# Kernel tuning notes

Measured on AMD Instinct MI355X. Metric: run time of the kernel, lower is better.

The kernel has to match this reference:

```python
import jax, jax.numpy as jnp
import numpy as np

B, T, H, CD, NC, S, D = 128, 256, 512, 128, 2048, 256, 9
EPS = 1e-5

def _lin(x, w, b):
    return x @ w.T + b

def _gru_cell(x, h, wih, whh, bih, bhh):
    gi = x @ wih.T + bih
    gh = h @ whh.T + bhh
    ir, iz, inn = jnp.split(gi, 3, axis=-1)
    hr, hz, hn = jnp.split(gh, 3, axis=-1)
    r = jax.nn.sigmoid(ir + hr)
    z = jax.nn.sigmoid(iz + hz)
    n = jnp.tanh(inn + r * hn)
    return (1.0 - z) * n + z * h

def _bn(x, g, b, m, v):
    # eval-mode BatchNorm1d over channel dim of [B,C,W]
    return (x - m[:, None]) * (g * jax.lax.rsqrt(v + EPS))[:, None] + b[:, None]

def _conv(x, w, b, stride, pad):
    y = jax.lax.conv_general_dilated(x, w, (stride,), [(pad, pad)], dimension_numbers=('NCW', 'OIW', 'NCW'))
    return y + b[:, None]

def _convT(x, w, b, stride, pad, out_pad):
    # torch ConvTranspose1d with weight [I,O,k] == dilated conv with flipped, transposed kernel
    k = w.shape[-1]
    w2 = jnp.flip(w, -1).transpose(1, 0, 2)  # [O,I,k]
    y = jax.lax.conv_general_dilated(x, w2, (1,), [(k - 1 - pad, k - 1 - pad + out_pad)], lhs_dilation=(stride,), dimension_numbers=('NCW', 'OIW', 'NCW'))
    return y + b[:, None]

def _gru_seq(x, h0, wih, whh, bih, bhh, reverse=False):
    def step(h, xt):
        hn = _gru_cell(xt, h, wih, whh, bih, bhh)
        return hn, hn
    _, ys = jax.lax.scan(step, h0, jnp.swapaxes(x, 0, 1), reverse=reverse)
    return jnp.swapaxes(ys, 0, 1)

def _forward(note, skel, skel_encoded, ehw, ehb, ifw, ifb, gfwih, gfwhh, gfbih, gfbhh, gbwih, gbwhh, gbbih, gbbhh, bn0g, bn0b, bn0m, bn0v, c1w, c1b, bn1g, bn1b, bn1m, bn1v, c2w, c2b, bn2g, bn2b, bn2m, bn2v, c3w, c3b, embed, ct1w, ct1b, dbn1g, dbn1b, dbn1m, dbn1v, ct2w, ct2b, dbn2g, dbn2b, dbn2m, dbn2v, dhw, dhb, g1wih, g1whh, g1bih, g1bhh, g2wih, g2whh, g2bih, g2bhh, nfw, nfb, samp_rand):
    sg = jax.lax.stop_gradient
    # ---- encoder ----
    hid = _lin(skel_encoded, ehw, ehb)                         # [B,H] shared init for both GRU dirs
    x = _lin(note, ifw, ifb)                                   # [B,T,H]
    fwd = _gru_seq(x, hid, gfwih, gfwhh, gfbih, gfbhh)
    bwd = _gru_seq(x, hid, gbwih, gbwhh, gbbih, gbbhh, reverse=True)
    out = jnp.concatenate([fwd, bwd], axis=-1).transpose(0, 2, 1)  # [B,2H,T]
    out = _bn(out, bn0g, bn0b, bn0m, bn0v)
    out = jax.nn.leaky_relu(_bn(_conv(out, c1w, c1b, 2, 1), bn1g, bn1b, bn1m, bn1v), 0.2)
    out = jax.nn.leaky_relu(_bn(_conv(out, c2w, c2b, 2, 1), bn2g, bn2b, bn2m, bn2v), 0.2)
    z = _conv(out, c3w, c3b, 1, 0)                             # [B,CD,T//4]
    # ---- vector quantizer (eval: no EMA update) ----
    zt = z.transpose(0, 2, 1)                                  # [B,T//4,CD]
    flat = zt.reshape(-1, CD)
    dist = (flat * flat).sum(1, keepdims=True) - 2.0 * flat @ embed.T + (embed * embed).sum(1)
    idx = jnp.argmin(dist, axis=1)                             # [B*T//4]
    quant = embed[idx].reshape(zt.shape)
    codebook_loss = jnp.mean((sg(quant) - zt) ** 2)
    cmt_loss = jnp.mean((quant - sg(zt)) ** 2)
    loss = codebook_loss + 0.2 * cmt_loss
    quant_st = zt + sg(quant - zt)                             # straight-through
    qz = quant_st.transpose(0, 2, 1)                           # [B,CD,T//4]
    avg_probs = jnp.zeros((NC,), zt.dtype).at[idx].add(1.0) / idx.shape[0]
    perplexity = jnp.exp(-jnp.sum(avg_probs * jnp.log(avg_probs + 1e-10)))
    enc_idx = idx.reshape(B, -1, 1)
    # ---- decoder ----
    d = jax.nn.leaky_relu(_bn(_convT(qz, ct1w, ct1b, 2, 0, 1), dbn1g, dbn1b, dbn1m, dbn1v), 0.2)
    d = jax.nn.leaky_relu(_bn(_convT(d, ct2w, ct2b, 2, 0, 0), dbn2g, dbn2b, dbn2m, dbn2v), 0.2)
    dec_in = d.transpose(0, 2, 1)                              # [B,T+8,H//2]
    h1 = _lin(skel_encoded, dhw, dhb)
    out0 = jnp.zeros((B, D), zt.dtype)
    cat0 = jnp.concatenate([out0, dec_in[:, 0], skel[:, 0]], axis=-1)
    h1 = _gru_cell(cat0, h1, g1wih, g1whh, g1bih, g1bhh)
    h2 = _gru_cell(h1, h1, g2wih, g2whh, g2bih, g2bhh)         # hx[1] init = hx[0] at i==0
    logit0 = _lin(h2, nfw, nfb)
    fb0 = (jax.nn.sigmoid(logit0) - samp_rand[0] > 0).astype(zt.dtype)  # eval-mode bernoulli sample
    def step(carry, xs):
        fb, h1, h2 = carry
        inp_i, skel_i, rand_i = xs
        h1 = _gru_cell(jnp.concatenate([fb, inp_i, skel_i], axis=-1), h1, g1wih, g1whh, g1bih, g1bhh)
        h2 = _gru_cell(h1, h2, g2wih, g2whh, g2bih, g2bhh)
        logits = _lin(h2, nfw, nfb)
        fb = (jax.nn.sigmoid(logits) - rand_i > 0).astype(logits.dtype)
        return (fb, h1, h2), logits
    xs = (jnp.swapaxes(dec_in[:, 1:T], 0, 1), jnp.swapaxes(skel[:, 1:T], 0, 1), samp_rand[1:T])
    _, logits_rest = jax.lax.scan(step, (fb0, h1, h2), xs)
    note_recon = jnp.swapaxes(jnp.concatenate([logit0[None], logits_rest], axis=0), 0, 1)  # [B,T,D]
    return note_recon, qz, loss, cmt_loss, enc_idx, perplexity

def setup_inputs():
    key = jax.random.key(0)
    ks = iter(jax.random.split(key, 96))
    nrm = lambda *s: jax.random.normal(next(ks), s, jnp.float32) * 0.05
    uni = lambda *s: jax.random.uniform(next(ks), s, jnp.float32)
    def bnp(c):
        g = 1.0 + 0.1 * jax.random.normal(next(ks), (c,), jnp.float32)
        b = nrm(c)
        m = nrm(c) * 2.0
        v = jax.random.uniform(next(ks), (c,), jnp.float32, 0.5, 1.5)
        return g, b, m, v
    inp = {}
    inp['note'] = uni(B, T, D)
    inp['skel'] = uni(B, T, D)
    inp['skel_encoded'] = jax.random.normal(next(ks), (B, S), jnp.float32)
    inp['ehw'] = nrm(H, S); inp['ehb'] = nrm(H)
    inp['ifw'] = nrm(H, D); inp['ifb'] = nrm(H)
    inp['gfwih'] = nrm(3 * H, H); inp['gfwhh'] = nrm(3 * H, H); inp['gfbih'] = nrm(3 * H); inp['gfbhh'] = nrm(3 * H)
    inp['gbwih'] = nrm(3 * H, H); inp['gbwhh'] = nrm(3 * H, H); inp['gbbih'] = nrm(3 * H); inp['gbbhh'] = nrm(3 * H)
    inp['bn0g'], inp['bn0b'], inp['bn0m'], inp['bn0v'] = bnp(2 * H)
    inp['c1w'] = nrm(H, 2 * H, 4); inp['c1b'] = nrm(H)
    inp['bn1g'], inp['bn1b'], inp['bn1m'], inp['bn1v'] = bnp(H)
    inp['c2w'] = nrm(H, H, 4); inp['c2b'] = nrm(H)
    inp['bn2g'], inp['bn2b'], inp['bn2m'], inp['bn2v'] = bnp(H)
    inp['c3w'] = nrm(CD, H, 1); inp['c3b'] = nrm(CD)
    inp['embed'] = jax.random.normal(next(ks), (NC, CD), jnp.float32)  # torch normal_() init, std 1
    inp['ct1w'] = nrm(CD, H, 4); inp['ct1b'] = nrm(H)
    inp['dbn1g'], inp['dbn1b'], inp['dbn1m'], inp['dbn1v'] = bnp(H)
    inp['ct2w'] = nrm(H, H // 2, 4); inp['ct2b'] = nrm(H // 2)
    inp['dbn2g'], inp['dbn2b'], inp['dbn2m'], inp['dbn2v'] = bnp(H // 2)
    inp['dhw'] = nrm(H, S); inp['dhb'] = nrm(H)
    inp['g1wih'] = nrm(3 * H, H // 2 + 2 * D); inp['g1whh'] = nrm(3 * H, H); inp['g1bih'] = nrm(3 * H); inp['g1bhh'] = nrm(3 * H)
    inp['g2wih'] = nrm(3 * H, H); inp['g2whh'] = nrm(3 * H, H); inp['g2bih'] = nrm(3 * H); inp['g2bhh'] = nrm(3 * H)
    inp['nfw'] = nrm(D, H); inp['nfb'] = nrm(D)
    inp['samp_rand'] = uni(T, B, D)  # pre-drawn noise for eval-mode bernoulli sampling
    inp['training'] = 0
    inp['teacher_forcing_ratio'] = 0
    return inp

def reference(note, skel, skel_encoded, ehw, ehb, ifw, ifb, gfwih, gfwhh, gfbih, gfbhh, gbwih, gbwhh, gbbih, gbbhh, bn0g, bn0b, bn0m, bn0v, c1w, c1b, bn1g, bn1b, bn1m, bn1v, c2w, c2b, bn2g, bn2b, bn2m, bn2v, c3w, c3b, embed, ct1w, ct1b, dbn1g, dbn1b, dbn1m, dbn1v, ct2w, ct2b, dbn2g, dbn2b, dbn2m, dbn2v, dhw, dhb, g1wih, g1whh, g1bih, g1bhh, g2wih, g2whh, g2bih, g2bhh, nfw, nfb, samp_rand, training, teacher_forcing_ratio):
    # eval path: training flag unused (dropout off, BN running stats, no EMA, always sample)
    return _forward(note, skel, skel_encoded, ehw, ehb, ifw, ifb, gfwih, gfwhh, gfbih, gfbhh, gbwih, gbwhh, gbbih, gbbhh, bn0g, bn0b, bn0m, bn0v, c1w, c1b, bn1g, bn1b, bn1m, bn1v, c2w, c2b, bn2g, bn2b, bn2m, bn2v, c3w, c3b, embed, ct1w, ct1b, dbn1g, dbn1b, dbn1m, dbn1v, ct2w, ct2b, dbn2g, dbn2b, dbn2m, dbn2v, dhw, dhb, g1wih, g1whh, g1bih, g1bhh, g2wih, g2whh, g2bih, g2bhh, nfw, nfb, samp_rand)
```

## Files before the change

kernel.cpp:

```cpp
#include <hip/hip_runtime.h>
#include <math.h>


#define DI __device__ __forceinline__

#define O_HF   ((size_t)0)
#define O_HB   ((size_t)131072)
#define O_H1   ((size_t)262144)
#define O_H2   ((size_t)393216)
#define O_WEFF ((size_t)524288)
#define O_BEFF ((size_t)551936)
#define O_BNS  ((size_t)555008)
#define O_ESQ  ((size_t)560640)
#define O_HIST ((size_t)562688)
#define O_RED  ((size_t)564736)
#define O_LOG  ((size_t)564752)
#define O_IDX  ((size_t)567056)
#define O_ZT   ((size_t)575248)
#define O_QT   ((size_t)1623824)
#define O_C2   ((size_t)2672400)
#define O_C1   ((size_t)6866704)
#define O_WT1  ((size_t)15255312)
#define O_WT2  ((size_t)17352464)
#define O_WT3  ((size_t)18401040)
// ... 51 lines not shown
  C0 = MF(A1,Q1,C0); C1 = MF(A1,Q0,C1); \
  C0 = MF(A0,Q2,C0); C1 = MF(A2,Q0,C1); \
  C0 = MF(A2,Q1,C0); C1 = MF(A1,Q2,C1);

#define FMA44 \
  acc[0][0] += a4.x*b4.x; acc[0][1] += a4.x*b4.y; acc[0][2] += a4.x*b4.z; acc[0][3] += a4.x*b4.w; \
  acc[1][0] += a4.y*b4.x; acc[1][1] += a4.y*b4.y; acc[1][2] += a4.y*b4.z; acc[1][3] += a4.y*b4.w; \
  acc[2][0] += a4.z*b4.x; acc[2][1] += a4.z*b4.y; acc[2][2] += a4.z*b4.z; acc[2][3] += a4.z*b4.w; \
  acc[3][0] += a4.w*b4.x; acc[3][1] += a4.w*b4.y; acc[3][2] += a4.w*b4.z; acc[3][3] += a4.w*b4.w;

__global__ void trans_kern(const float* __restrict__ c1w, const float* __restrict__ c2w,
                           const float* __restrict__ c3w, const float* __restrict__ ct1w,
                           const float* __restrict__ ct2w, float* __restrict__ ws){
  const int A1 = 2097152, A2 = 3145728, A3 = 3211264, A4 = 3473408, A5 = 3997696;
  for (int i = blockIdx.x*256 + threadIdx.x; i < A5; i += gridDim.x*256){
    if (i < A1){
      int j = i; int oc = j & 511; int t = j >> 9; int ic = t & 1023; int k = t >> 10;
      ws[O_WT1 + j] = c1w[((size_t)oc*1024 + ic)*4 + k];
    } else if (i < A2){
      int j = i - A1; int oc = j & 511; int t = j >> 9; int ic = t & 511; int k = t >> 9;
      ws[O_WT2 + j] = c2w[((size_t)oc*512 + ic)*4 + k];
    } else if (i < A3){
      int j = i - A2; int oc = j & 127; int ic = j >> 7;
      ws[O_WT3 + j] = c3w[(size_t)oc*512 + ic];
    } else if (i < A4){
      int j = i - A3; int oc = j & 511; int t = j >> 9; int ic = t & 127; int k = t >> 7;
      ws[O_WTD1 + j] = ct1w[((size_t)ic*512 + oc)*4 + k];
    } else {
      int j = i - A4; int oc = j & 255; int t = j >> 8; int ic = t & 511; int k = t >> 9;
      ws[O_WTD2 + j] = ct2w[((size_t)ic*256 + oc)*4 + k];
    }
  }
}

__global__ void bn_kern(const float* g0,const float* b0,const float* m0,const float* v0,
                        const float* g1,const float* b1,const float* m1,const float* v1,
                        const float* g2,const float* b2,const float* m2,const float* v2,
                        const float* gd1,const float* bd1,const float* md1,const float* vd1,
                        const float* gd2,const float* bd2,const float* md2,const float* vd2,
                        float* __restrict__ bns){
  int i = blockIdx.x*256 + threadIdx.x;
  if (i >= 2816) return;
  const float *g,*b,*m,*v; int c, so, to;
  if (i < 1024){ g=g0;b=b0;m=m0;v=v0;c=i;so=BN0S;to=BN0T; }
  else if (i < 1536){ g=g1;b=b1;m=m1;v=v1;c=i-1024;so=BN1S;to=BN1T; }
  else if (i < 2048){ g=g2;b=b2;m=m2;v=v2;c=i-1536;so=BN2S;to=BN2T; }
  else if (i < 2560){ g=gd1;b=bd1;m=md1;v=vd1;c=i-2048;so=DB1S;to=DB1T; }
  else              { g=gd2;b=bd2;m=md2;v=vd2;c=i-2560;so=DB2S;to=DB2T; }
  float s = g[c]*rsqrtf(v[c] + 1e-5f);
  bns[so + c] = s;
  bns[to + c] = b[c] - m[c]*s;
}

__global__ __launch_bounds__(256) void init_kern(const float* __restrict__ se,
    const float* __restrict__ ehw, const float* __restrict__ ehb,
    const float* __restrict__ dhw, const float* __restrict__ dhb, float* __restrict__ ws){
  int idx = blockIdx.x*256 + threadIdx.x;
  int n = idx & 1023, b = idx >> 10;
  const float* w; float bias;
  if (n < 512){ w = ehw + (size_t)n*256; bias = ehb[n]; }
  else        { w = dhw + (size_t)(n-512)*256; bias = dhb[n-512]; }
  const float* sp = se + (size_t)b*256;
  float acc = bias;
  for (int k = 0; k < 256; ++k) acc += sp[k]*w[k];
  if (n < 512){
    ws[O_HF + 65536 + b*512 + n] = acc;
    ws[O_HB + 65536 + b*512 + n] = acc;
    unsigned short s0,s1,s2; split3(acc, s0,s1,s2);
    unsigned short* esh = (unsigned short*)(ws + ESOFF) + 4718592;
    int off = 196608 + b*512 + n;
    esh[off] = s0; esh[off+65536] = s1; esh[off+131072] = s2;
    esh[393216+off] = s0; esh[393216+off+65536] = s1; esh[393216+off+131072] = s2;
  } else {
    ws[O_H1 + 65536 + b*512 + (n-512)] = acc;
  }
}

__global__ __launch_bounds__(256) void weff_kern(const float* __restrict__ gfwih,
    const float* __restrict__ gfbih, const float* __restrict__ gbwih, const float* __restrict__ gbbih,
    const float* __restrict__ ifw, const float* __restrict__ ifb, float* __restrict__ ws){
  int idx = blockIdx.x*256 + threadIdx.x;
  if (idx >= 30720) return;
  int dir = idx / 15360; int r = idx - dir*15360;
  int j3 = r / 10; int d = r - j3*10;
  const float* wih = dir ? gbwih : gfwih;
  float acc = 0.f;
  if (d < 9){
    for (int k = 0; k < 512; ++k) acc += wih[(size_t)j3*512 + k]*ifw[k*9 + d];
    ws[O_WEFF + dir*13824 + j3*9 + d] = acc;
  } else {
    for (int k = 0; k < 512; ++k) acc += wih[(size_t)j3*512 + k]*ifb[k];
    acc += (dir ? gbbih : gfbih)[j3];
    ws[O_BEFF + dir*1536 + j3] = acc;
  }
}

__global__ __launch_bounds__(256) void esq_kern(const float* __restrict__ embed, float* __restrict__ ws){
  int e = blockIdx.x*256 + threadIdx.x;
  float acc = 0.f;
  for (int c = 0; c < 128; ++c){ float t = embed[(size_t)e*128 + c]; acc += t*t; }
  ws[O_ESQ + e] = acc;
  if (blockIdx.x == 0){
    for (int i = threadIdx.x; i < 2048; i += 256) ws[O_HIST + i] = 0.f;
    if (threadIdx.x < 16) ws[O_RED + threadIdx.x] = 0.f;
  }
}

__global__ void split_w_kern(const float* __restrict__ gfwhh,
    const float* __restrict__ gbwhh, float* __restrict__ ws){
  unsigned short* es = (unsigned short*)(ws + ESOFF);
  for (int i = blockIdx.x*256 + threadIdx.x; i < 1572864; i += gridDim.x*256){
    int half = i >= 786432;
    int idx = i - (half ? 786432 : 0);
    float x = half ? gbwhh[idx] : gfwhh[idx];
    unsigned short s0,s1,s2; split3(x,s0,s1,s2);
    unsigned short* d = es + (half ? 2359296 : 0);
    d[idx] = s0; d[idx+786432] = s1; d[idx+1572864] = s2;
  }
}

__global__ void split_w2_kern(const float* __restrict__ g1wih, const float* __restrict__ g1whh,
    const float* __restrict__ g2wih, const float* __restrict__ g2whh, float* __restrict__ ws){
  unsigned short* dsb = (unsigned short*)(ws + DSOFF);
  const int total = 393216 + 3*786432 + 65536;
  for (int i = blockIdx.x*256 + threadIdx.x; i < total; i += gridDim.x*256){
    float x; unsigned short* d; int off, stride;
    if (i < 393216){
      int row = i>>8, k = i&255;
      x = g1wih[(size_t)row*274 + 9 + k]; d = dsb; off = i; stride = 393216;
    } else if (i < 1179648){
      int idx = i-393216; x = g1whh[idx]; d = dsb + 1179648; off = idx; stride = 786432;
    } else if (i < 1966080){
      int idx = i-1179648; x = g2wih[idx]; d = dsb + 3538944; off = idx; stride = 786432;
    } else if (i < 2752512){
      int idx = i-1966080; x = g2whh[idx]; d = dsb + 5898240; off = idx; stride = 786432;
    } else {
      int idx = i-2752512; x = ws[O_H1 + 65536 + idx];
      d = dsb + 8257536 + 196608; off = idx; stride = 65536;
    }
    unsigned short s0,s1,s2; split3(x,s0,s1,s2);
    d[off] = s0; d[off+stride] = s1; d[off+2*stride] = s2;
  }
}

__global__ void split_dec_kern(float* __restrict__ ws){
  unsigned short* decs = (unsigned short*)(ws + ESOFF);
  const float* dec = ws + O_DEC;
  for (int i = blockIdx.x*256 + threadIdx.x; i < 8388608; i += gridDim.x*256){
    unsigned short s0,s1,s2; split3(dec[i],s0,s1,s2);
    decs[i] = s0; decs[i+8388608] = s1; decs[i+16777216] = s2;
  }
}

__global__ __launch_bounds__(256) void enc_step_mfma(
    float* __restrict__ ws, const float* __restrict__ note,
    const float* __restrict__ gfbhh, const float* __restrict__ gbbhh, int step){
  int bi = blockIdx.x;
  int dir = bi>>7, bt = (bi>>5)&3, jt = bi&31;
  int b0 = bt*32, j0 = jt*16;
  int tid = threadIdx.x, w = tid>>6, l = tid&63;
  int m = w&1, kh = w>>1;
  int pb = (step+1)&1, cb = step&1;
  float* hprev = ws + (dir? O_HB : O_HF) + (size_t)pb*65536;
  float* hnext = ws + (dir? O_HB : O_HF) + (size_t)cb*65536;
  unsigned short* esh = (unsigned short*)(ws + ESOFF) + 4718592 + dir*393216;
  const unsigned short* hsp = esh + pb*196608;
  unsigned short* hsn = esh + cb*196608;
  const unsigned short* wsp = (const unsigned short*)(ws + ESOFF) + dir*2359296;
  const float* weff = ws + O_WEFF + dir*13824;
  const float* beff = ws + O_BEFF + dir*1536;
  const float* bhh = dir? gbbhh : gfbhh;
  const float* bns = ws + O_BNS;
  float* ys = ws + O_YS;

  const unsigned short* ab = hsp + (b0 + m*16 + (l&15))*512 + kh*256 + ((l>>4)<<3);
  const unsigned short* bb = wsp + (j0 + (l&15))*512 + kh*256 + ((l>>4)<<3);
  f32x4 z4 = {0.f,0.f,0.f,0.f};
  f32x4 acc[3][2] = {{z4,z4},{z4,z4},{z4,z4}};
  #pragma unroll
  for (int kt = 0; kt < 8; ++kt){
    s8v a0 = LD8(ab + kt*32);
    s8v a1 = LD8(ab + 65536 + kt*32);
    s8v a2 = LD8(ab + 131072 + kt*32);
    #pragma unroll
    for (int g = 0; g < 3; ++g){
      const unsigned short* bp = bb + g*262144 + kt*32;
      s8v q0 = LD8(bp);
      s8v q1 = LD8(bp + 786432);
      s8v q2 = LD8(bp + 1572864);
      MF8(a0,a1,a2, q0,q1,q2, acc[g][0], acc[g][1])
    }
  }
  __shared__ float red[3072];
  #pragma unroll
  for (int g = 0; g < 3; ++g){
    f32x4 s = acc[g][0] + acc[g][1];
    #pragma unroll
    for (int i = 0; i < 4; ++i) red[((w*3+g)<<8) + (i<<6) + l] = s[i];
  }
  __syncthreads();
  int t = dir ? 255-step : step;
  #pragma unroll
  for (int ii = 0; ii < 2; ++ii){
    int i = kh*2 + ii;
    int b = b0 + m*16 + ((l>>4)<<2) + i;
    int j = j0 + (l&15);
    float Y[3];
    #pragma unroll
    for (int g = 0; g < 3; ++g)
      Y[g] = red[((m*3+g)<<8)+(i<<6)+l] + red[((m*3+g+6)<<8)+(i<<6)+l];
    const float* nt = note + ((size_t)b*256 + t)*9;
    float gi[3];
    #pragma unroll
    for (int g = 0; g < 3; ++g){
      const float* wr = weff + (size_t)(g*512+j)*9;
      float a = beff[g*512+j];
      #pragma unroll
      for (int d = 0; d < 9; ++d) a += nt[d]*wr[d];
      gi[g] = a;
    }
    float hpv = hprev[(size_t)b*512 + j];
    float r = sigm(gi[0] + Y[0] + bhh[j]);
    float zz = sigm(gi[1] + Y[1] + bhh[512+j]);
    float nn = tanhf(gi[2] + r*(Y[2] + bhh[1024+j]));
    float h = (1.f - zz)*nn + zz*hpv;
    hnext[(size_t)b*512 + j] = h;
    unsigned short s0,s1,s2; split3(h, s0,s1,s2);
    int off = b*512 + j;
    hsn[off] = s0; hsn[off+65536] = s1; hsn[off+131072] = s2;
    int c = dir*512 + j;
    ys[((size_t)b*256 + t)*1024 + c] = h*bns[BN0S + c] + bns[BN0T + c];
  }
}

__global__ __launch_bounds__(256) void dec_k1_mfma(
    float* __restrict__ ws, const float* __restrict__ skel, const float* __restrict__ sr,
    const float* __restrict__ w1ih, const float* __restrict__ b1ih,
    const float* __restrict__ b1hh, const float* __restrict__ nfb,
    float* __restrict__ dout, int step){
  int bi = blockIdx.x;
  int bt = bi>>5, jt = bi&31;
  int b0 = bt*16, j0 = jt*16;
  int tid = threadIdx.x, w = tid>>6, l = tid&63;
  int kh = w;
  int pb = (step+1)&1, cb = step&1;
  const float* h1p = ws + O_H1 + (size_t)pb*65536;
  float* h1n = ws + O_H1 + (size_t)cb*65536;
  const float* logp = ws + O_LOG + (size_t)pb*1152;
  float* logc = ws + O_LOG + (size_t)cb*1152;
  unsigned short* dsb = (unsigned short*)(ws + DSOFF);
  const unsigned short* h1sp = dsb + 8257536 + pb*196608;
  unsigned short* h1sn = dsb + 8257536 + cb*196608;
  const unsigned short* decs = (const unsigned short*)(ws + ESOFF);
  const unsigned short* w1d = dsb;
  const unsigned short* w1h = dsb + 1179648;

  __shared__ float fbs[144], ssh[144];
  __shared__ float red[6144];
  if (tid < 144){
    int bb = tid/9, d = tid - bb*9; int b = b0 + bb;
    float fv = 0.f;
    if (step > 0){
      float lg = logp[b*9 + d];
      fv = (1.f/(1.f + expf(-lg)) - sr[(size_t)(step-1)*1152 + b*9 + d]) > 0.f ? 1.f : 0.f;
    }
    fbs[tid] = fv;
    ssh[tid] = skel[((size_t)b*256 + step)*9 + d];
  }
  if (bi == 0){
    for (int idx = tid; idx < 1152; idx += 256){
      logc[idx] = nfb[idx % 9];
      if (step > 0) dout[OUT_NR + (size_t)(idx/9)*2304 + (step-1)*9 + (idx%9)] = logp[idx];
    }
  }
  f32x4 z4 = {0.f,0.f,0.f,0.f};
  f32x4 gia[3][2] = {{z4,z4},{z4,z4},{z4,z4}};
  f32x4 gha[3][2] = {{z4,z4},{z4,z4},{z4,z4}};
  {
    const unsigned short* ab = decs + (b0 + (l&15))*65536 + step*256 + kh*64 + ((l>>4)<<3);
    const unsigned short* bb = w1d + (j0 + (l&15))*256 + kh*64 + ((l>>4)<<3);
    #pragma unroll
    for (int kt = 0; kt < 2; ++kt){
      s8v a0 = LD8(ab + kt*32);
      s8v a1 = LD8(ab + 8388608 + kt*32);
      s8v a2 = LD8(ab + 16777216 + kt*32);
      #pragma unroll
      for (int g = 0; g < 3; ++g){
        const unsigned short* bp = bb + g*131072 + kt*32;
        s8v q0 = LD8(bp);
        s8v q1 = LD8(bp + 393216);
        s8v q2 = LD8(bp + 786432);
        MF8(a0,a1,a2, q0,q1,q2, gia[g][0], gia[g][1])
      }
    }
  }
  {
    const unsigned short* ab = h1sp + (b0 + (l&15))*512 + kh*128 + ((l>>4)<<3);
    const unsigned short* bb = w1h + (j0 + (l&15))*512 + kh*128 + ((l>>4)<<3);
    #pragma unroll
    for (int kt = 0; kt < 4; ++kt){
      s8v a0 = LD8(ab + kt*32);
      s8v a1 = LD8(ab + 65536 + kt*32);
      s8v a2 = LD8(ab + 131072 + kt*32);
      #pragma unroll
      for (int g = 0; g < 3; ++g){
        const unsigned short* bp = bb + g*262144 + kt*32;
        s8v q0 = LD8(bp);
        s8v q1 = LD8(bp + 786432);
        s8v q2 = LD8(bp + 1572864);
        MF8(a0,a1,a2, q0,q1,q2, gha[g][0], gha[g][1])
      }
    }
  }
  #pragma unroll
  for (int g = 0; g < 3; ++g){
    f32x4 s = gia[g][0] + gia[g][1];
    f32x4 t = gha[g][0] + gha[g][1];
    #pragma unroll
    for (int i = 0; i < 4; ++i){
      red[((w*6+g)<<8) + (i<<6) + l] = s[i];
      red[((w*6+g+3)<<8) + (i<<6) + l] = t[i];
    }
  }
  __syncthreads();
  int i = w;
  int b = b0 + ((l>>4)<<2) + i;
  int j = j0 + (l&15);
  float GI[3], GH[3];
  #pragma unroll
  for (int pg = 0; pg < 3; ++pg){
    float a = 0.f, c = 0.f;
    #pragma unroll
    for (int ww = 0; ww < 4; ++ww){
      a += red[((ww*6+pg)<<8)+(i<<6)+l];
      c += red[((ww*6+pg+3)<<8)+(i<<6)+l];
    }
    GI[pg] = a; GH[pg] = c;
  }
  int bb = b - b0;
  #pragma unroll
  for (int g = 0; g < 3; ++g){
    const float* wr = w1ih + (size_t)(g*512+j)*274;
    float a = GI[g] + b1ih[g*512+j];
    #pragma unroll
    for (int d = 0; d < 9; ++d) a += fbs[bb*9+d]*wr[d] + ssh[bb*9+d]*wr[265+d];
    GI[g] = a;
  }
  float hpv = h1p[(size_t)b*512 + j];
  float r = sigm(GI[0] + GH[0] + b1hh[j]);
  float zz = sigm(GI[1] + GH[1] + b1hh[512+j]);
  float nn = tanhf(GI[2] + r*(GH[2] + b1hh[1024+j]));
  float h = (1.f-zz)*nn + zz*hpv;
  h1n[(size_t)b*512 + j] = h;
  unsigned short s0,s1,s2; split3(h,s0,s1,s2);
  int off = b*512 + j;
  h1sn[off] = s0; h1sn[off+65536] = s1; h1sn[off+131072] = s2;
}

__global__ __launch_bounds__(256) void dec_k2_mfma(
    float* __restrict__ ws, const float* __restrict__ b2ih, const float* __restrict__ b2hh,
    const float* __restrict__ nfw, int step){
  int bi = blockIdx.x;
  int bt = bi>>5, jt = bi&31;
  int b0 = bt*16, j0 = jt*16;
  int tid = threadIdx.x, w = tid>>6, l = tid&63;
  int kh = w;
  int pb = (step+1)&1, cb = step&1;
  const float* h1n = ws + O_H1 + (size_t)cb*65536;
  const float* h2p = (step==0) ? h1n : ws + O_H2 + (size_t)pb*65536;
  float* h2n = ws + O_H2 + (size_t)cb*65536;
  float* logc = ws + O_LOG + (size_t)cb*1152;
  unsigned short* dsb = (unsigned short*)(ws + DSOFF);
  const unsigned short* h1sn = dsb + 8257536 + cb*196608;
  const unsigned short* h2sp = (step==0) ? h1sn : dsb + 8650752 + pb*196608;
  unsigned short* h2sn = dsb + 8650752 + cb*196608;
  const unsigned short* w2i = dsb + 3538944;
  const unsigned short* w2h = dsb + 5898240;

  __shared__ float red[6144];
  __shared__ float hsm[256];
  f32x4 z4 = {0.f,0.f,0.f,0.f};
  f32x4 gia[3][2] = {{z4,z4},{z4,z4},{z4,z4}};
  f32x4 gha[3][2] = {{z4,z4},{z4,z4},{z4,z4}};
  {
    const unsigned short* ab = h1sn + (b0 + (l&15))*512 + kh*128 + ((l>>4)<<3);
    const unsigned short* bb = w2i + (j0 + (l&15))*512 + kh*128 + ((l>>4)<<3);
    #pragma unroll
    for (int kt = 0; kt < 4; ++kt){
      s8v a0 = LD8(ab + kt*32);
      s8v a1 = LD8(ab + 65536 + kt*32);
      s8v a2 = LD8(ab + 131072 + kt*32);
      #pragma unroll
      for (int g = 0; g < 3; ++g){
        const unsigned short* bp = bb + g*262144 + kt*32;
        s8v q0 = LD8(bp);
        s8v q1 = LD8(bp + 786432);
        s8v q2 = LD8(bp + 1572864);
        MF8(a0,a1,a2, q0,q1,q2, gia[g][0], gia[g][1])
      }
    }
  }
  {
    const unsigned short* ab = h2sp + (b0 + (l&15))*512 + kh*128 + ((l>>4)<<3);
    const unsigned short* bb = w2h + (j0 + (l&15))*512 + kh*128 + ((l>>4)<<3);
    #pragma unroll
    for (int kt = 0; kt < 4; ++kt){
      s8v a0 = LD8(ab + kt*32);
      s8v a1 = LD8(ab + 65536 + kt*32);
      s8v a2 = LD8(ab + 131072 + kt*32);
      #pragma unroll
      for (int g = 0; g < 3; ++g){
        const unsigned short* bp = bb + g*262144 + kt*32;
        s8v q0 = LD8(bp);
        s8v q1 = LD8(bp + 786432);
        s8v q2 = LD8(bp + 1572864);
        MF8(a0,a1,a2, q0,q1,q2, gha[g][0], gha[g][1])
      }
    }
  }
  #pragma unroll
  for (int g = 0; g < 3; ++g){
    f32x4 s = gia[g][0] + gia[g][1];
    f32x4 t = gha[g][0] + gha[g][1];
    #pragma unroll
    for (int i = 0; i < 4; ++i){
      red[((w*6+g)<<8) + (i<<6) + l] = s[i];
      red[((w*6+g+3)<<8) + (i<<6) + l] = t[i];
    }
  }
  __syncthreads();
  int i = w;
  int b = b0 + ((l>>4)<<2) + i;
  int j = j0 + (l&15);
  float GI[3], GH[3];
  #pragma unroll
  for (int pg = 0; pg < 3; ++pg){
    float a = 0.f, c = 0.f;
    #pragma unroll
    for (int ww = 0; ww < 4; ++ww){
      a += red[((ww*6+pg)<<8)+(i<<6)+l];
      c += red[((ww*6+pg+3)<<8)+(i<<6)+l];
    }
    GI[pg] = a; GH[pg] = c;
  }
  float hpv = h2p[(size_t)b*512 + j];
  float r = sigm(GI[0] + b2ih[j] + GH[0] + b2hh[j]);
  float zz = sigm(GI[1] + b2ih[512+j] + GH[1] + b2hh[512+j]);
  float nn = tanhf(GI[2] + b2ih[1024+j] + r*(GH[2] + b2hh[1024+j]));
  float h = (1.f-zz)*nn + zz*hpv;
  h2n[(size_t)b*512 + j] = h;
  unsigned short s0,s1,s2; split3(h,s0,s1,s2);
  int off = b*512 + j;
  h2sn[off] = s0; h2sn[off+65536] = s1; h2sn[off+131072] = s2;
  hsm[(b-b0)*16 + (j-j0)] = h;
  __syncthreads();
  if (tid < 144){
    int bq = tid/9, d = tid - bq*9;
    float v = 0.f;
    #pragma unroll
    for (int jl = 0; jl < 16; ++jl) v += hsm[bq*16+jl]*nfw[(size_t)d*512 + j0 + jl];
    atomicAdd(&logc[(b0+bq)*9 + d], v);
  }
}

__global__ __launch_bounds__(256) void conv1_kern(const float* __restrict__ ysb,
    const float* __restrict__ wt, const float* __restrict__ cb,
    const float* __restrict__ bns, float* __restrict__ outp){
  int gm = blockIdx.x, gn = blockIdx.y;
  int b = gm >> 1, ot0 = (gm & 1) << 6, oc0 = gn << 6;
  int tid = threadIdx.x, tx = tid & 15, ty = tid >> 4;
  __shared__ __align__(16) float As[32*68];
  __shared__ __align__(16) float Bs[32*68];
  float acc[4][4] = {};
  for (int k = 0; k < 4; ++k){
    for (int ic0 = 0; ic0 < 1024; ic0 += 32){
      #pragma unroll
      for (int rr = 0; rr < 8; ++rr){
        int e = rr*256 + tid; int m = e >> 5, ic = e & 31;
        int tin = ((ot0 + m) << 1) + k - 1;
        float v = 0.f;
        if ((unsigned)tin < 256u) v = ysb[((size_t)b*256 + tin)*1024 + ic0 + ic];
        As[ic*68 + m] = v;
      }
      #pragma unroll
      for (int rr = 0; rr < 8; ++rr){
        int e = rr*256 + tid; int oc = e & 63, ic = e >> 6;
        Bs[ic*68 + oc] = wt[((size_t)k*1024 + ic0 + ic)*512 + oc0 + oc];
      }
      __syncthreads();
      #pragma unroll
      for (int kk = 0; kk < 32; ++kk){
        float4 a4 = *(const float4*)&As[kk*68 + ty*4];
        float4 b4 = *(const float4*)&Bs[kk*68 + tx*4];
        FMA44
      }
      __syncthreads();
    }
  }
  #pragma unroll
  for (int i = 0; i < 4; ++i){
    int ot = ot0 + ty*4 + i;
    #pragma unroll
    for (int jj = 0; jj < 4; ++jj){
      int oc = oc0 + tx*4 + jj;
      float v = acc[i][jj] + cb[oc];
      v = v*bns[BN1S + oc] + bns[BN1T + oc];
      v = v > 0.f ? v : 0.2f*v;
      outp[((size_t)b*128 + ot)*512 + oc] = v;
    }
  }
}

__global__ __launch_bounds__(256) void conv2_kern(const float* __restrict__ c1o,
    const float* __restrict__ wt, const float* __restrict__ cb,
    const float* __restrict__ bns, float* __restrict__ outp){
  int b = blockIdx.x, oc0 = blockIdx.y << 6;
  int tid = threadIdx.x, tx = tid & 15, ty = tid >> 4;
  __shared__ __align__(16) float As[32*68];
  __shared__ __align__(16) float Bs[32*68];
  float acc[4][4] = {};
  for (int k = 0; k < 4; ++k){
    for (int ic0 = 0; ic0 < 512; ic0 += 32){
      #pragma unroll
      for (int rr = 0; rr < 8; ++rr){
        int e = rr*256 + tid; int m = e >> 5, ic = e & 31;
        int tin = (m << 1) + k - 1;
        float v = 0.f;
        if ((unsigned)tin < 128u) v = c1o[((size_t)b*128 + tin)*512 + ic0 + ic];
        As[ic*68 + m] = v;
      }
      #pragma unroll
      for (int rr = 0; rr < 8; ++rr){
        int e = rr*256 + tid; int oc = e & 63, ic = e >> 6;
        Bs[ic*68 + oc] = wt[((size_t)k*512 + ic0 + ic)*512 + oc0 + oc];
      }
      __syncthreads();
      #pragma unroll
      for (int kk = 0; kk < 32; ++kk){
        float4 a4 = *(const float4*)&As[kk*68 + ty*4];
        float4 b4 = *(const float4*)&Bs[kk*68 + tx*4];
        FMA44
      }
      __syncthreads();
    }
  }
  #pragma unroll
  for (int i = 0; i < 4; ++i){
    int ot = ty*4 + i;
    #pragma unroll
    for (int jj = 0; jj < 4; ++jj){
      int oc = oc0 + tx*4 + jj;
      float v = acc[i][jj] + cb[oc];
      v = v*bns[BN2S + oc] + bns[BN2T + oc];
      v = v > 0.f ? v : 0.2f*v;
      outp[((size_t)b*64 + ot)*512 + oc] = v;
    }
  }
}

__global__ __launch_bounds__(256) void conv3_kern(const float* __restrict__ c2o,
    const float* __restrict__ wt, const float* __restrict__ cb, float* __restrict__ zt){
  int row0 = blockIdx.x << 6, oc0 = blockIdx.y << 6;
  int tid = threadIdx.x, tx = tid & 15, ty = tid >> 4;
  __shared__ __align__(16) float As[32*68];
  __shared__ __align__(16) float Bs[32*68];
  float acc[4][4] = {};
  for (int ic0 = 0; ic0 < 512; ic0 += 32){
    #pragma unroll
    for (int rr = 0; rr < 8; ++rr){
      int e = rr*256 + tid; int m = e >> 5, ic = e & 31;
      As[ic*68 + m] = c2o[((size_t)(row0 + m))*512 + ic0 + ic];
    }
    #pragma unroll
    for (int rr = 0; rr < 8; ++rr){
      int e = rr*256 + tid; int oc = e & 63, ic = e >> 6;
      Bs[ic*68 + oc] = wt[(size_t)(ic0 + ic)*128 + oc0 + oc];
    }
    __syncthreads();
    #pragma unroll
    for (int kk = 0; kk < 32; ++kk){
      float4 a4 = *(const float4*)&As[kk*68 + ty*4];
      float4 b4 = *(const float4*)&Bs[kk*68 + tx*4];
      FMA44
    }
    __syncthreads();
  }
  #pragma unroll
  for (int i = 0; i < 4; ++i){
    int row = row0 + ty*4 + i;
    #pragma unroll
    for (int jj = 0; jj < 4; ++jj){
      int oc = oc0 + tx*4 + jj;
      zt[(size_t)row*128 + oc] = acc[i][jj] + cb[oc];
    }
  }
}

__global__ __launch_bounds__(256) void vq_kern(const float* __restrict__ zt,
    const float* __restrict__ esq, const float* __restrict__ embed,
    int* __restrict__ idxp, float* __restrict__ hist, float* __restrict__ dout){
  int r0 = blockIdx.x * 8;
  int tid = threadIdx.x;
  int r = tid >> 5, el = tid & 31;
  __shared__ __align__(16) float zsh[1024];
  __shared__ __align__(16) float esh[4096];
  __shared__ float rv[256]; __shared__ int ri[256];
  for (int idx = tid; idx < 1024; idx += 256) zsh[idx] = zt[(size_t)r0*128 + idx];
// ... 113 lines not shown
      }
      __syncthreads();
    }
  }
  #pragma unroll
  for (int i = 0; i < 4; ++i){
    int op = op0 + ty*4 + i;
    #pragma unroll
    for (int jj = 0; jj < 4; ++jj){
      int oc = oc0 + tx*4 + jj;
      float v = acc[i][jj] + cb[oc];
      v = v*bns[DB1S + oc] + bns[DB1T + oc];
      v = v > 0.f ? v : 0.2f*v;
      d1[((size_t)b*128 + op)*512 + oc] = v;
    }
  }
}

__global__ __launch_bounds__(256) void convt2_kern(const float* __restrict__ d1,
    const float* __restrict__ wt, const float* __restrict__ cb,
    const float* __restrict__ bns, float* __restrict__ dec){
  int gm = blockIdx.x;
  int b = gm >> 2, op0 = (gm & 3) << 6, oc0 = blockIdx.y << 6;
  int tid = threadIdx.x, tx = tid & 15, ty = tid >> 4;
  __shared__ __align__(16) float As[32*68];
  __shared__ __align__(16) float Bs[32*68];
  float acc[4][4] = {};
  for (int k = 0; k < 4; ++k){
    for (int ic0 = 0; ic0 < 512; ic0 += 32){
      #pragma unroll
      for (int rr = 0; rr < 8; ++rr){
        int e = rr*256 + tid; int m = e >> 5, ic = e & 31;
        int op = op0 + m;
        float v = 0.f;
        if (op >= k && (((op - k) & 1) == 0)){
          int ip = (op - k) >> 1;
          v = d1[((size_t)b*128 + ip)*512 + ic0 + ic];
        }
        As[ic*68 + m] = v;
      }
      #pragma unroll
      for (int rr = 0; rr < 8; ++rr){
        int e = rr*256 + tid; int oc = e & 63, ic = e >> 6;
        Bs[ic*68 + oc] = wt[((size_t)k*512 + ic0 + ic)*256 + oc0 + oc];
      }
      __syncthreads();
      #pragma unroll
      for (int kk = 0; kk < 32; ++kk){
        float4 a4 = *(const float4*)&As[kk*68 + ty*4];
        float4 b4 = *(const float4*)&Bs[kk*68 + tx*4];
        FMA44
      }
      __syncthreads();
    }
  }
  #pragma unroll
  for (int i = 0; i < 4; ++i){
    int op = op0 + ty*4 + i;
    #pragma unroll
    for (int jj = 0; jj < 4; ++jj){
      int oc = oc0 + tx*4 + jj;
      float v = acc[i][jj] + cb[oc];
      v = v*bns[DB2S + oc] + bns[DB2T + oc];
      v = v > 0.f ? v : 0.2f*v;
      dec[((size_t)b*256 + op)*256 + oc] = v;
    }
  }
}

__global__ void copylast_kern(const float* __restrict__ logit1, float* __restrict__ dout){
  int idx = blockIdx.x*256 + threadIdx.x;
  if (idx < 1152) dout[OUT_NR + (size_t)(idx/9)*2304 + 255*9 + (idx % 9)] = logit1[idx];
}

extern "C" void kernel_launch(void* const* d_in, const int* in_sizes, int n_in,
                              void* d_out, int out_size, void* d_ws, size_t ws_size,
                              hipStream_t stream){
  (void)in_sizes; (void)n_in; (void)out_size; (void)ws_size;
  const float* note  = (const float*)d_in[0];
  const float* skel  = (const float*)d_in[1];
  const float* se    = (const float*)d_in[2];
  const float* ehw   = (const float*)d_in[3];
  const float* ehb   = (const float*)d_in[4];
  const float* ifw   = (const float*)d_in[5];
  const float* ifb   = (const float*)d_in[6];
  const float* gfwih = (const float*)d_in[7];
  const float* gfwhh = (const float*)d_in[8];
  const float* gfbih = (const float*)d_in[9];
  const float* gfbhh = (const float*)d_in[10];
  const float* gbwih = (const float*)d_in[11];
  const float* gbwhh = (const float*)d_in[12];
  const float* gbbih = (const float*)d_in[13];
  const float* gbbhh = (const float*)d_in[14];
  const float* bn0g  = (const float*)d_in[15];
  const float* bn0b  = (const float*)d_in[16];
  const float* bn0m  = (const float*)d_in[17];
  const float* bn0v  = (const float*)d_in[18];
  const float* c1w   = (const float*)d_in[19];
  const float* c1b   = (const float*)d_in[20];
  const float* bn1g  = (const float*)d_in[21];
  const float* bn1b  = (const float*)d_in[22];
  const float* bn1m  = (const float*)d_in[23];
  const float* bn1v  = (const float*)d_in[24];
  const float* c2w   = (const float*)d_in[25];
  const float* c2b   = (const float*)d_in[26];
  const float* bn2g  = (const float*)d_in[27];
  const float* bn2b  = (const float*)d_in[28];
  const float* bn2m  = (const float*)d_in[29];
  const float* bn2v  = (const float*)d_in[30];
  const float* c3w   = (const float*)d_in[31];
  const float* c3b   = (const float*)d_in[32];
  const float* embed = (const float*)d_in[33];
  const float* ct1w  = (const float*)d_in[34];
  const float* ct1b  = (const float*)d_in[35];
  const float* dbn1g = (const float*)d_in[36];
  const float* dbn1b = (const float*)d_in[37];
  const float* dbn1m = (const float*)d_in[38];
  const float* dbn1v = (const float*)d_in[39];
  const float* ct2w  = (const float*)d_in[40];
  const float* ct2b  = (const float*)d_in[41];
  const float* dbn2g = (const float*)d_in[42];
  const float* dbn2b = (const float*)d_in[43];
  const float* dbn2m = (const float*)d_in[44];
  const float* dbn2v = (const float*)d_in[45];
  const float* dhw   = (const float*)d_in[46];
  const float* dhb   = (const float*)d_in[47];
  const float* g1wih = (const float*)d_in[48];
  const float* g1whh = (const float*)d_in[49];
  const float* g1bih = (const float*)d_in[50];
  const float* g1bhh = (const float*)d_in[51];
  const float* g2wih = (const float*)d_in[52];
  const float* g2whh = (const float*)d_in[53];
  const float* g2bih = (const float*)d_in[54];
  const float* g2bhh = (const float*)d_in[55];
  const float* nfw   = (const float*)d_in[56];
  const float* nfb   = (const float*)d_in[57];
  const float* sr    = (const float*)d_in[58];

  float* ws  = (float*)d_ws;
  float* out = (float*)d_out;
  float* ysp  = ws + O_YS;
  float* bnsp = ws + O_BNS;

  trans_kern<<<dim3(2048), dim3(256), 0, stream>>>(c1w, c2w, c3w, ct1w, ct2w, ws);
  bn_kern<<<dim3(11), dim3(256), 0, stream>>>(bn0g,bn0b,bn0m,bn0v, bn1g,bn1b,bn1m,bn1v,
                                              bn2g,bn2b,bn2m,bn2v, dbn1g,dbn1b,dbn1m,dbn1v,
                                              dbn2g,dbn2b,dbn2m,dbn2v, bnsp);
  init_kern<<<dim3(512), dim3(256), 0, stream>>>(se, ehw, ehb, dhw, dhb, ws);
  weff_kern<<<dim3(120), dim3(256), 0, stream>>>(gfwih, gfbih, gbwih, gbbih, ifw, ifb, ws);
  esq_kern<<<dim3(8), dim3(256), 0, stream>>>(embed, ws);
  split_w_kern<<<dim3(1024), dim3(256), 0, stream>>>(gfwhh, gbwhh, ws);

  for (int s = 0; s < 256; ++s){
    enc_step_mfma<<<dim3(256), dim3(256), 0, stream>>>(ws, note, gfbhh, gbbhh, s);
  }

  conv1_kern<<<dim3(256, 8), dim3(256), 0, stream>>>(ysp, ws + O_WT1, c1b, bnsp, ws + O_C1);
  split_w2_kern<<<dim3(2048), dim3(256), 0, stream>>>(g1wih, g1whh, g2wih, g2whh, ws);
  conv2_kern<<<dim3(128, 8), dim3(256), 0, stream>>>(ws + O_C1, ws + O_WT2, c2b, bnsp, ws + O_C2);
  conv3_kern<<<dim3(128, 2), dim3(256), 0, stream>>>(ws + O_C2, ws + O_WT3, c3b, ws + O_ZT);

  vq_kern<<<dim3(1024), dim3(256), 0, stream>>>(ws + O_ZT, ws + O_ESQ, embed,
      (int*)(ws + O_IDX), ws + O_HIST, out);
  quant_kern<<<dim3(1024), dim3(256), 0, stream>>>(ws + O_ZT, (const int*)(ws + O_IDX),
      embed, ws + O_QT, ws + O_RED, out);
  perp_kern<<<dim3(1), dim3(256), 0, stream>>>(ws + O_HIST, ws + O_RED, out);

  convt1_kern<<<dim3(256, 8), dim3(256), 0, stream>>>(ws + O_QT, ws + O_WTD1, ct1b, bnsp, ws + O_D1);
  convt2_kern<<<dim3(512, 4), dim3(256), 0, stream>>>(ws + O_D1, ws + O_WTD2, ct2b, bnsp, ws + O_DEC);
  split_dec_kern<<<dim3(2048), dim3(256), 0, stream>>>(ws);

  for (int i = 0; i < 256; ++i){
    dec_k1_mfma<<<dim3(256), dim3(256), 0, stream>>>(ws, skel, sr, g1wih, g1bih,
        g1bhh, nfb, out, i);
    dec_k2_mfma<<<dim3(256), dim3(256), 0, stream>>>(ws, g2bih, g2bhh, nfw, i);
  }
  copylast_kern<<<dim3(5), dim3(256), 0, stream>>>(ws + O_LOG + 1152, out);
}
```

Measured before the change: 14.94 ms.

## Double waves per block in recurrent GRU step kernels via finer K-split

Result: faster. 14.50 ms (-3.0%).

```diff
diff --git a/kernel.cpp b/kernel.cpp
--- a/kernel.cpp
+++ b/kernel.cpp
@@ -227,14 +227,14 @@
   }
 }
 
-__global__ __launch_bounds__(256) void enc_step_mfma(
+__global__ __launch_bounds__(512) void enc_step_mfma(
     float* __restrict__ ws, const float* __restrict__ note,
     const float* __restrict__ gfbhh, const float* __restrict__ gbbhh, int step){
   int bi = blockIdx.x;
   int dir = bi>>7, bt = (bi>>5)&3, jt = bi&31;
   int b0 = bt*32, j0 = jt*16;
   int tid = threadIdx.x, w = tid>>6, l = tid&63;
-  int m = w&1, kh = w>>1;
+  int m = w&1, kq = w>>1;
   int pb = (step+1)&1, cb = step&1;
   float* hprev = ws + (dir? O_HB : O_HF) + (size_t)pb*65536;
   float* hnext = ws + (dir? O_HB : O_HF) + (size_t)cb*65536;
@@ -248,12 +248,12 @@
   const float* bns = ws + O_BNS;
   float* ys = ws + O_YS;
 
-  const unsigned short* ab = hsp + (b0 + m*16 + (l&15))*512 + kh*256 + ((l>>4)<<3);
-  const unsigned short* bb = wsp + (j0 + (l&15))*512 + kh*256 + ((l>>4)<<3);
+  const unsigned short* ab = hsp + (size_t)(b0 + m*16 + (l&15))*512 + kq*128 + ((l>>4)<<3);
+  const unsigned short* bb = wsp + (size_t)(j0 + (l&15))*512 + kq*128 + ((l>>4)<<3);
   f32x4 z4 = {0.f,0.f,0.f,0.f};
   f32x4 acc[3][2] = {{z4,z4},{z4,z4},{z4,z4}};
   #pragma unroll
-  for (int kt = 0; kt < 8; ++kt){
+  for (int kt = 0; kt < 4; ++kt){
     s8v a0 = LD8(ab + kt*32);
     s8v a1 = LD8(ab + 65536 + kt*32);
     s8v a2 = LD8(ab + 131072 + kt*32);
@@ -266,7 +266,7 @@
       MF8(a0,a1,a2, q0,q1,q2, acc[g][0], acc[g][1])
     }
   }
-  __shared__ float red[3072];
+  __shared__ float red[6144];
   #pragma unroll
   for (int g = 0; g < 3; ++g){
     f32x4 s = acc[g][0] + acc[g][1];
@@ -275,40 +275,42 @@
   }
   __syncthreads();
   int t = dir ? 255-step : step;
-  #pragma unroll
-  for (int ii = 0; ii < 2; ++ii){
-    int i = kh*2 + ii;
-    int b = b0 + m*16 + ((l>>4)<<2) + i;
-    int j = j0 + (l&15);
-    float Y[3];
-    #pragma unroll
-    for (int g = 0; g < 3; ++g)
-      Y[g] = red[((m*3+g)<<8)+(i<<6)+l] + red[((m*3+g+6)<<8)+(i<<6)+l];
-    const float* nt = note + ((size_t)b*256 + t)*9;
-    float gi[3];
-    #pragma unroll
-    for (int g = 0; g < 3; ++g){
-      const float* wr = weff + (size_t)(g*512+j)*9;
-      float a = beff[g*512+j];
-      #pragma unroll
-      for (int d = 0; d < 9; ++d) a += nt[d]*wr[d];
-      gi[g] = a;
-    }
-    float hpv = hprev[(size_t)b*512 + j];
-    float r = sigm(gi[0] + Y[0] + bhh[j]);
-    float zz = sigm(gi[1] + Y[1] + bhh[512+j]);
-    float nn = tanhf(gi[2] + r*(Y[2] + bhh[1024+j]));
-    float h = (1.f - zz)*nn + zz*hpv;
-    hnext[(size_t)b*512 + j] = h;
-    unsigned short s0,s1,s2; split3(h, s0,s1,s2);
-    int off = b*512 + j;
-    hsn[off] = s0; hsn[off+65536] = s1; hsn[off+131072] = s2;
-    int c = dir*512 + j;
-    ys[((size_t)b*256 + t)*1024 + c] = h*bns[BN0S + c] + bns[BN0T + c];
-  }
-}
-
-__global__ __launch_bounds__(256) void dec_k1_mfma(
+  int i = kq;
+  int b = b0 + m*16 + ((l>>4)<<2) + i;
+  int j = j0 + (l&15);
+  float Y[3];
+  #pragma unroll
+  for (int g = 0; g < 3; ++g){
+    float y = 0.f;
+    #pragma unroll
+    for (int q = 0; q < 4; ++q)
+      y += red[(((m + 2*q)*3 + g)<<8) + (i<<6) + l];
+    Y[g] = y;
+  }
+  const float* nt = note + ((size_t)b*256 + t)*9;
+  float gi[3];
+  #pragma unroll
+  for (int g = 0; g < 3; ++g){
+    const float* wr = weff + (size_t)(g*512+j)*9;
+    float a = beff[g*512+j];
+    #pragma unroll
+    for (int d = 0; d < 9; ++d) a += nt[d]*wr[d];
+    gi[g] = a;
+  }
+  float hpv = hprev[(size_t)b*512 + j];
+  float r = sigm(gi[0] + Y[0] + bhh[j]);
+  float zz = sigm(gi[1] + Y[1] + bhh[512+j]);
+  float nn = tanhf(gi[2] + r*(Y[2] + bhh[1024+j]));
+  float h = (1.f - zz)*nn + zz*hpv;
+  hnext[(size_t)b*512 + j] = h;
+  unsigned short s0,s1,s2; split3(h, s0,s1,s2);
+  int off = b*512 + j;
+  hsn[off] = s0; hsn[off+65536] = s1; hsn[off+131072] = s2;
+  int c = dir*512 + j;
+  ys[((size_t)b*256 + t)*1024 + c] = h*bns[BN0S + c] + bns[BN0T + c];
+}
+
+__global__ __launch_bounds__(512) void dec_k1_mfma(
     float* __restrict__ ws, const float* __restrict__ skel, const float* __restrict__ sr,
     const float* __restrict__ w1ih, const float* __restrict__ b1ih,
     const float* __restrict__ b1hh, const float* __restrict__ nfb,
@@ -317,7 +319,6 @@
   int bt = bi>>5, jt = bi&31;
   int b0 = bt*16, j0 = jt*16;
   int tid = threadIdx.x, w = tid>>6, l = tid&63;
-  int kh = w;
   int pb = (step+1)&1, cb = step&1;
   const float* h1p = ws + O_H1 + (size_t)pb*65536;
   float* h1n = ws + O_H1 + (size_t)cb*65536;
@@ -331,19 +332,19 @@
   const unsigned short* w1h = dsb + 1179648;
 
   __shared__ float fbs[144], ssh[144];
-  __shared__ float red[6144];
+  __shared__ float red[12288];
   if (tid < 144){
     int bb = tid/9, d = tid - bb*9; int b = b0 + bb;
     float fv = 0.f;
     if (step > 0){
       float lg = logp[b*9 + d];
-      fv = (1.f/(1.f + expf(-lg)) - sr[(size_t)(step-1)*1152 + b*9 + d]) > 0.f ? 1.f : 0.f;
+      fv = (sigm(lg) - sr[(size_t)(step-1)*1152 + b*9 + d]) > 0.f ? 1.f : 0.f;
     }
     fbs[tid] = fv;
     ssh[tid] = skel[((size_t)b*256 + step)*9 + d];
   }
   if (bi == 0){
-    for (int idx = tid; idx < 1152; idx += 256){
+    for (int idx = tid; idx < 1152; idx += 512){
       logc[idx] = nfb[idx % 9];
       if (step > 0) dout[OUT_NR + (size_t)(idx/9)*2304 + (step-1)*9 + (idx%9)] = logp[idx];
     }
@@ -352,34 +353,31 @@
   f32x4 gia[3][2] = {{z4,z4},{z4,z4},{z4,z4}};
   f32x4 gha[3][2] = {{z4,z4},{z4,z4},{z4,z4}};
   {
-    const unsigned short* ab = decs + (b0 + (l&15))*65536 + step*256 + kh*64 + ((l>>4)<<3);
-    const unsigned short* bb = w1d + (j0 + (l&15))*256 + kh*64 + ((l>>4)<<3);
+    const unsigned short* ab = decs + (size_t)(b0 + (l&15))*65536 + step*256 + w*32 + ((l>>4)<<3);
+    const unsigned short* bbp = w1d + (size_t)(j0 + (l&15))*256 + w*32 + ((l>>4)<<3);
+    s8v a0 = LD8(ab);
+    s8v a1 = LD8(ab + 8388608);
+    s8v a2 = LD8(ab + 16777216);
+    #pragma unroll
+    for (int g = 0; g < 3; ++g){
+      const unsigned short* bp = bbp + g*131072;
+      s8v q0 = LD8(bp);
+      s8v q1 = LD8(bp + 393216);
+      s8v q2 = LD8(bp + 786432);
+      MF8(a0,a1,a2, q0,q1,q2, gia[g][0], gia[g][1])
+    }
+  }
+  {
+    const unsigned short* ab = h1sp + (size_t)(b0 + (l&15))*512 + w*64 + ((l>>4)<<3);
+    const unsigned short* bbp = w1h + (size_t)(j0 + (l&15))*512 + w*64 + ((l>>4)<<3);
     #pragma unroll
     for (int kt = 0; kt < 2; ++kt){
-      s8v a0 = LD8(ab + kt*32);
-      s8v a1 = LD8(ab + 8388608 + kt*32);
-      s8v a2 = LD8(ab + 16777216 + kt*32);
-      #pragma unroll
-      for (int g = 0; g < 3; ++g){
-        const unsigned short* bp = bb + g*131072 + kt*32;
-        s8v q0 = LD8(bp);
-        s8v q1 = LD8(bp + 393216);
-        s8v q2 = LD8(bp + 786432);
-        MF8(a0,a1,a2, q0,q1,q2, gia[g][0], gia[g][1])
-      }
-    }
-  }
-  {
-    const unsigned short* ab = h1sp + (b0 + (l&15))*512 + kh*128 + ((l>>4)<<3);
-    const unsigned short* bb = w1h + (j0 + (l&15))*512 + kh*128 + ((l>>4)<<3);
-    #pragma unroll
-    for (int kt = 0; kt < 4; ++kt){
       s8v a0 = LD8(ab + kt*32);
       s8v a1 = LD8(ab + 65536 + kt*32);
       s8v a2 = LD8(ab + 131072 + kt*32);
       #pragma unroll
       for (int g = 0; g < 3; ++g){
-        const unsigned short* bp = bb + g*262144 + kt*32;
+        const unsigned short* bp = bbp + g*262144 + kt*32;
         s8v q0 = LD8(bp);
         s8v q1 = LD8(bp + 786432);
         s8v q2 = LD8(bp + 1572864);
@@ -398,48 +396,49 @@
     }
   }
   __syncthreads();
-  int i = w;
-  int b = b0 + ((l>>4)<<2) + i;
-  int j = j0 + (l&15);
-  float GI[3], GH[3];
-  #pragma unroll
-  for (int pg = 0; pg < 3; ++pg){
-    float a = 0.f, c = 0.f;
-    #pragma unroll
-    for (int ww = 0; ww < 4; ++ww){
-      a += red[((ww*6+pg)<<8)+(i<<6)+l];
-      c += red[((ww*6+pg+3)<<8)+(i<<6)+l];
-    }
-    GI[pg] = a; GH[pg] = c;
-  }
-  int bb = b - b0;
-  #pragma unroll
-  for (int g = 0; g < 3; ++g){
-    const float* wr = w1ih + (size_t)(g*512+j)*274;
-    float a = GI[g] + b1ih[g*512+j];
-    #pragma unroll
-    for (int d = 0; d < 9; ++d) a += fbs[bb*9+d]*wr[d] + ssh[bb*9+d]*wr[265+d];
-    GI[g] = a;
-  }
-  float hpv = h1p[(size_t)b*512 + j];
-  float r = sigm(GI[0] + GH[0] + b1hh[j]);
-  float zz = sigm(GI[1] + GH[1] + b1hh[512+j]);
-  float nn = tanhf(GI[2] + r*(GH[2] + b1hh[1024+j]));
-  float h = (1.f-zz)*nn + zz*hpv;
-  h1n[(size_t)b*512 + j] = h;
-  unsigned short s0,s1,s2; split3(h,s0,s1,s2);
-  int off = b*512 + j;
-  h1sn[off] = s0; h1sn[off+65536] = s1; h1sn[off+131072] = s2;
-}
-
-__global__ __launch_bounds__(256) void dec_k2_mfma(
+  if (w < 4){
+    int i = w;
+    int b = b0 + ((l>>4)<<2) + i;
+    int j = j0 + (l&15);
+    float GI[3], GH[3];
+    #pragma unroll
+    for (int pg = 0; pg < 3; ++pg){
+      float a = 0.f, c = 0.f;
+      #pragma unroll
+      for (int ww = 0; ww < 8; ++ww){
+        a += red[((ww*6+pg)<<8)+(i<<6)+l];
+        c += red[((ww*6+pg+3)<<8)+(i<<6)+l];
+      }
+      GI[pg] = a; GH[pg] = c;
+    }
+    int bb = b - b0;
+    #pragma unroll
+    for (int g = 0; g < 3; ++g){
+      const float* wr = w1ih + (size_t)(g*512+j)*274;
+      float a = GI[g] + b1ih[g*512+j];
+      #pragma unroll
+      for (int d = 0; d < 9; ++d) a += fbs[bb*9+d]*wr[d] + ssh[bb*9+d]*wr[265+d];
+      GI[g] = a;
+    }
+    float hpv = h1p[(size_t)b*512 + j];
+    float r = sigm(GI[0] + GH[0] + b1hh[j]);
+    float zz = sigm(GI[1] + GH[1] + b1hh[512+j]);
+    float nn = tanhf(GI[2] + r*(GH[2] + b1hh[1024+j]));
+    float h = (1.f-zz)*nn + zz*hpv;
+    h1n[(size_t)b*512 + j] = h;
+    unsigned short s0,s1,s2; split3(h,s0,s1,s2);
+    int off = b*512 + j;
+    h1sn[off] = s0; h1sn[off+65536] = s1; h1sn[off+131072] = s2;
+  }
+}
+
+__global__ __launch_bounds__(512) void dec_k2_mfma(
     float* __restrict__ ws, const float* __restrict__ b2ih, const float* __restrict__ b2hh,
     const float* __restrict__ nfw, int step){
   int bi = blockIdx.x;
   int bt = bi>>5, jt = bi&31;
   int b0 = bt*16, j0 = jt*16;
   int tid = threadIdx.x, w = tid>>6, l = tid&63;
-  int kh = w;
   int pb = (step+1)&1, cb = step&1;
   const float* h1n = ws + O_H1 + (size_t)cb*65536;
   const float* h2p = (step==0) ? h1n : ws + O_H2 + (size_t)pb*65536;
@@ -452,22 +451,22 @@
   const unsigned short* w2i = dsb + 3538944;
   const unsigned short* w2h = dsb + 5898240;
 
-  __shared__ float red[6144];
+  __shared__ float red[12288];
   __shared__ float hsm[256];
   f32x4 z4 = {0.f,0.f,0.f,0.f};
   f32x4 gia[3][2] = {{z4,z4},{z4,z4},{z4,z4}};
   f32x4 gha[3][2] = {{z4,z4},{z4,z4},{z4,z4}};
   {
-    const unsigned short* ab = h1sn + (b0 + (l&15))*512 + kh*128 + ((l>>4)<<3);
-    const unsigned short* bb = w2i + (j0 + (l&15))*512 + kh*128 + ((l>>4)<<3);
-    #pragma unroll
-    for (int kt = 0; kt < 4; ++kt){
+    const unsigned short* ab = h1sn + (size_t)(b0 + (l&15))*512 + w*64 + ((l>>4)<<3);
+    const unsigned short* bbp = w2i + (size_t)(j0 + (l&15))*512 + w*64 + ((l>>4)<<3);
+    #pragma unroll
+    for (int kt = 0; kt < 2; ++kt){
       s8v a0 = LD8(ab + kt*32);
       s8v a1 = LD8(ab + 65536 + kt*32);
       s8v a2 = LD8(ab + 131072 + kt*32);
       #pragma unroll
       for (int g = 0; g < 3; ++g){
-        const unsigned short* bp = bb + g*262144 + kt*32;
+        const unsigned short* bp = bbp + g*262144 + kt*32;
         s8v q0 = LD8(bp);
         s8v q1 = LD8(bp + 786432);
         s8v q2 = LD8(bp + 1572864);
@@ -476,16 +475,16 @@
     }
   }
   {
-    const unsigned short* ab = h2sp + (b0 + (l&15))*512 + kh*128 + ((l>>4)<<3);
-    const unsigned short* bb = w2h + (j0 + (l&15))*512 + kh*128 + ((l>>4)<<3);
-    #pragma unroll
-    for (int kt = 0; kt < 4; ++kt){
+    const unsigned short* ab = h2sp + (size_t)(b0 + (l&15))*512 + w*64 + ((l>>4)<<3);
+    const unsigned short* bbp = w2h + (size_t)(j0 + (l&15))*512 + w*64 + ((l>>4)<<3);
+    #pragma unroll
+    for (int kt = 0; kt < 2; ++kt){
       s8v a0 = LD8(ab + kt*32);
       s8v a1 = LD8(ab + 65536 + kt*32);
       s8v a2 = LD8(ab + 131072 + kt*32);
       #pragma unroll
       for (int g = 0; g < 3; ++g){
-        const unsigned short* bp = bb + g*262144 + kt*32;
+        const unsigned short* bp = bbp + g*262144 + kt*32;
         s8v q0 = LD8(bp);
         s8v q1 = LD8(bp + 786432);
         s8v q2 = LD8(bp + 1572864);
@@ -504,30 +503,32 @@
     }
   }
   __syncthreads();
-  int i = w;
-  int b = b0 + ((l>>4)<<2) + i;
-  int j = j0 + (l&15);
-  float GI[3], GH[3];
-  #pragma unroll
-  for (int pg = 0; pg < 3; ++pg){
-    float a = 0.f, c = 0.f;
-    #pragma unroll
-    for (int ww = 0; ww < 4; ++ww){
-      a += red[((ww*6+pg)<<8)+(i<<6)+l];
-      c += red[((ww*6+pg+3)<<8)+(i<<6)+l];
-    }
-    GI[pg] = a; GH[pg] = c;
-  }
-  float hpv = h2p[(size_t)b*512 + j];
-  float r = sigm(GI[0] + b2ih[j] + GH[0] + b2hh[j]);
-  float zz = sigm(GI[1] + b2ih[512+j] + GH[1] + b2hh[512+j]);
-  float nn = tanhf(GI[2] + b2ih[1024+j] + r*(GH[2] + b2hh[1024+j]));
-  float h = (1.f-zz)*nn + zz*hpv;
-  h2n[(size_t)b*512 + j] = h;
-  unsigned short s0,s1,s2; split3(h,s0,s1,s2);
-  int off = b*512 + j;
-  h2sn[off] = s0; h2sn[off+65536] = s1; h2sn[off+131072] = s2;
-  hsm[(b-b0)*16 + (j-j0)] = h;
+  if (w < 4){
+    int i = w;
+    int b = b0 + ((l>>4)<<2) + i;
+    int j = j0 + (l&15);
+    float GI[3], GH[3];
+    #pragma unroll
+    for (int pg = 0; pg < 3; ++pg){
+      float a = 0.f, c = 0.f;
+      #pragma unroll
+      for (int ww = 0; ww < 8; ++ww){
+        a += red[((ww*6+pg)<<8)+(i<<6)+l];
+        c += red[((ww*6+pg+3)<<8)+(i<<6)+l];
+      }
+      GI[pg] = a; GH[pg] = c;
+    }
+    float hpv = h2p[(size_t)b*512 + j];
+    float r = sigm(GI[0] + b2ih[j] + GH[0] + b2hh[j]);
+    float zz = sigm(GI[1] + b2ih[512+j] + GH[1] + b2hh[512+j]);
+    float nn = tanhf(GI[2] + b2ih[1024+j] + r*(GH[2] + b2hh[1024+j]));
+    float h = (1.f-zz)*nn + zz*hpv;
+    h2n[(size_t)b*512 + j] = h;
+    unsigned short s0,s1,s2; split3(h,s0,s1,s2);
+    int off = b*512 + j;
+    h2sn[off] = s0; h2sn[off+65536] = s1; h2sn[off+131072] = s2;
+    hsm[(b-b0)*16 + (j-j0)] = h;
+  }
   __syncthreads();
   if (tid < 144){
     int bq = tid/9, d = tid - bq*9;
@@ -947,7 +948,7 @@
   split_w_kern<<<dim3(1024), dim3(256), 0, stream>>>(gfwhh, gbwhh, ws);
 
   for (int s = 0; s < 256; ++s){
-    enc_step_mfma<<<dim3(256), dim3(256), 0, stream>>>(ws, note, gfbhh, gbbhh, s);
+    enc_step_mfma<<<dim3(256), dim3(512), 0, stream>>>(ws, note, gfbhh, gbbhh, s);
   }
 
   conv1_kern<<<dim3(256, 8), dim3(256), 0, stream>>>(ysp, ws + O_WT1, c1b, bnsp, ws + O_C1);
@@ -966,9 +967,9 @@
   split_dec_kern<<<dim3(2048), dim3(256), 0, stream>>>(ws);
 
   for (int i = 0; i < 256; ++i){
-    dec_k1_mfma<<<dim3(256), dim3(256), 0, stream>>>(ws, skel, sr, g1wih, g1bih,
+    dec_k1_mfma<<<dim3(256), dim3(512), 0, stream>>>(ws, skel, sr, g1wih, g1bih,
         g1bhh, nfb, out, i);
-    dec_k2_mfma<<<dim3(256), dim3(256), 0, stream>>>(ws, g2bih, g2bhh, nfw, i);
+    dec_k2_mfma<<<dim3(256), dim3(512), 0, stream>>>(ws, g2bih, g2bhh, nfw, i);
   }
   copylast_kern<<<dim3(5), dim3(256), 0, stream>>>(ws + O_LOG + 1152, out);
 }
```
